# Kernel tuning notes

Hardware: AMD Instinct MI355X
Metric: run time of the kernel (lower is better)

Reference implementation:

```python
import jax, jax.numpy as jnp
import numpy as np

B, S, D, H, HD = 4, 2048, 1024, 16, 64  # batch, seq, d_model, heads, head_dim


def setup_inputs() -> dict:
    key = jax.random.key(0)
    ks = jax.random.split(key, 9)
    scale = 0.02
    x = jax.random.normal(ks[0], (B, S, D), jnp.float32)
    Wq = jax.random.normal(ks[1], (D, H, HD), jnp.float32) * scale
    Wk = jax.random.normal(ks[2], (D, H, HD), jnp.float32) * scale
    Wv = jax.random.normal(ks[3], (D, H, HD), jnp.float32) * scale
    bq = jax.random.normal(ks[4], (H, HD), jnp.float32) * scale
    bk = jax.random.normal(ks[5], (H, HD), jnp.float32) * scale
    bv = jax.random.normal(ks[6], (H, HD), jnp.float32) * scale
    Wo = jax.random.normal(ks[7], (H, HD, D), jnp.float32) * scale
    bo = jax.random.normal(ks[8], (D,), jnp.float32) * scale
    return {"x": x, "Wq": Wq, "bq": bq, "Wk": Wk, "bk": bk,
            "Wv": Wv, "bv": bv, "Wo": Wo, "bo": bo}


def reference(x, Wq, bq, Wk, bk, Wv, bv, Wo, bo):
    # QKV projections -> (B, S, H, HD)
    q = jnp.einsum("bsd,dhe->bshe", x, Wq) + bq
    k = jnp.einsum("bsd,dhe->bshe", x, Wk) + bk
    v = jnp.einsum("bsd,dhe->bshe", x, Wv) + bv
    # scaled dot-product attention (deterministic, no mask/bias)
    q = q / jnp.sqrt(jnp.asarray(HD, q.dtype))
    scores = jnp.einsum("bqhd,bkhd->bhqk", q, k)  # (B, H, S, S)
    attn = jax.nn.softmax(scores, axis=-1)
    ctx = jnp.einsum("bhqk,bkhd->bqhd", attn, v)  # (B, S, H, HD)
    # output projection -> (B, S, D)
    return jnp.einsum("bqhd,hdo->bqo", ctx, Wo) + bo
```

## Files before the change

### kernel.cpp

```cpp
#include <hip/hip_runtime.h>


typedef unsigned short u16;
typedef __attribute__((ext_vector_type(4))) float f32x4;
typedef __attribute__((ext_vector_type(8))) short s16x8;
typedef __attribute__((ext_vector_type(4))) unsigned short u16x4;
typedef __attribute__((ext_vector_type(4))) unsigned int u32x4;

#define DEV __device__ __forceinline__

#if __has_builtin(__builtin_amdgcn_exp2f)
#define EXP2(x) __builtin_amdgcn_exp2f(x)
#else
#define EXP2(x) exp2f(x)
#endif

DEV u16 f2b(float f) {
  unsigned u = __float_as_uint(f);
  u += 0x7fffu + ((u >> 16) & 1u);
  return (u16)(u >> 16);
}

DEV unsigned packb(float a, float b) {
  return (unsigned)f2b(a) | ((unsigned)f2b(b) << 16);
}

DEV void async16(const void* g, void* l) {
  __builtin_amdgcn_global_load_lds(
      (const __attribute__((address_space(1))) unsigned int*)g,
      (__attribute__((address_space(3))) unsigned int*)l, 16, 0, 0);
}

__global__ void k_cast(const float* __restrict__ x, u16* __restrict__ xb) {
  int i = (blockIdx.x * 256 + threadIdx.x) * 4;
  float4 v = *(const float4*)(x + i);
  u16x4 o;
  o.x = f2b(v.x); o.y = f2b(v.y); o.z = f2b(v.z); o.w = f2b(v.w);
  *(u16x4*)(xb + i) = o;
}

__global__ void k_packw(const float* __restrict__ src, u16* __restrict__ dst, float scale) {
  __shared__ float tile[32][33];
  int t = threadIdx.x;
  int k0 = blockIdx.x * 32, n0 = blockIdx.y * 32;
  int c = t & 31, r0 = t >> 5;
#pragma unroll
  for (int p = 0; p < 4; ++p) {
    int r = p * 8 + r0;
    tile[r][c] = src[(size_t)(k0 + r) * 1024 + n0 + c] * scale;
  }
  __syncthreads();
#pragma unroll
  for (int p = 0; p < 4; ++p) {
    int r = p * 8 + r0;
    dst[(size_t)(n0 + r) * 1024 + k0 + c] = f2b(tile[c][r]);
  }
}

__global__ void k_packbias(const float* __restrict__ bq, const float* __restrict__ bk,
                           const float* __restrict__ bv, float* __restrict__ out,
                           float qscale) {
  int t = blockIdx.x * 256 + threadIdx.x;
  float v = (t < 1024) ? bq[t] * qscale : (t < 2048 ? bk[t - 1024] : bv[t - 2048]);
  out[t] = v;
}

template <bool OUT_BF16>
__global__ __launch_bounds__(256, 2) void k_gemm_bt(
    const u16* __restrict__ A, const u16* __restrict__ Bt,
    const float* __restrict__ bias, void* __restrict__ Cout, u16* __restrict__ VT,
    int K, int ldC, int nsplit) {
  __shared__ u16 As[128 * 64];
  __shared__ u16 Bs[128 * 64];
  const int t = threadIdx.x;
  const int w = t >> 6, l = t & 63;
  const int lane15 = l & 15, quad = l >> 4;
  const int m0 = blockIdx.x * 128, n0 = blockIdx.y * 128;
  const int wm = (w >> 1) * 64, wn = (w & 1) * 64;

  const int srow = t >> 3, cp = t & 7;
  const u16* aSrc[4]; const u16* bSrc[4]; int ldsOff[4];
#pragma unroll
  for (int i = 0; i < 4; ++i) {
    int row = i * 32 + srow;
    int gc = cp ^ (row & 7);
    aSrc[i] = A + (size_t)(m0 + row) * K + gc * 8;
    bSrc[i] = Bt + (size_t)(n0 + row) * K + gc * 8;
    ldsOff[i] = (i * 32 + w * 8) * 64;
  }

  f32x4 acc[4][4] = {};

  for (int kk = 0; kk < K; kk += 64) {
#pragma unroll
    for (int i = 0; i < 4; ++i) async16(aSrc[i] + kk, As + ldsOff[i]);
#pragma unroll
    for (int i = 0; i < 4; ++i) async16(bSrc[i] + kk, Bs + ldsOff[i]);
    __builtin_amdgcn_s_waitcnt(0);
    __syncthreads();

#pragma unroll
    for (int ks = 0; ks < 2; ++ks) {
      s16x8 af[4], bf[4];
#pragma unroll
      for (int mi = 0; mi < 4; ++mi) {
        int r = wm + mi * 16 + lane15;
        int c = ks * 4 + quad;
        af[mi] = *(const s16x8*)(As + r * 64 + (c ^ (r & 7)) * 8);
      }
#pragma unroll
      for (int ni = 0; ni < 4; ++ni) {
        int r = wn + ni * 16 + lane15;
        int c = ks * 4 + quad;
        bf[ni] = *(const s16x8*)(Bs + r * 64 + (c ^ (r & 7)) * 8);
      }
#pragma unroll
      for (int mi = 0; mi < 4; ++mi)
#pragma unroll
        for (int ni = 0; ni < 4; ++ni)
          acc[mi][ni] = __builtin_amdgcn_mfma_f32_16x16x32_bf16(af[mi], bf[ni], acc[mi][ni], 0, 0, 0);
    }
    __syncthreads();
  }

  const bool vpath = (VT != nullptr) && (n0 >= nsplit);
#pragma unroll
  for (int ni = 0; ni < 4; ++ni) {
    int gn = n0 + wn + ni * 16 + lane15;
    float bb = bias[gn];
    if (!vpath) {
#pragma unroll
      for (int mi = 0; mi < 4; ++mi) {
        int gmBase = m0 + wm + mi * 16 + quad * 4;
#pragma unroll
        for (int r = 0; r < 4; ++r) {
          float v = acc[mi][ni][r] + bb;
          if (OUT_BF16)
            ((u16*)Cout)[(size_t)(gmBase + r) * ldC + gn] = f2b(v);
          else
            ((float*)Cout)[(size_t)(gmBase + r) * ldC + gn] = v;
        }
      }
    } else {
      int gv = gn - nsplit;
      int hh = gv >> 6, hd = gv & 63;
#pragma unroll
      for (int mi = 0; mi < 4; ++mi) {
        int gmBase = m0 + wm + mi * 16 + quad * 4;
        int bb2 = gmBase >> 11, s = gmBase & 2047;
        u16x4 o;
        o.x = f2b(acc[mi][ni][0] + bb);
        o.y = f2b(acc[mi][ni][1] + bb);
        o.z = f2b(acc[mi][ni][2] + bb);
        o.w = f2b(acc[mi][ni][3] + bb);
        *(u16x4*)(VT + (((size_t)(bb2 * 16 + hh) * 64 + hd) * 2048 + s)) = o;
      }
    }
  }
}

__global__ __launch_bounds__(256, 6) void k_flash(
    const u16* __restrict__ qkv, const u16* __restrict__ vt, u16* __restrict__ ctx) {
  __shared__ u16 Ks[64 * 64];
  __shared__ u16 Vs[64 * 64];
  const int t = threadIdx.x;
  const int w = t >> 6, l = t & 63;
  const int lane15 = l & 15, quad = l >> 4;
  const int qt = blockIdx.x, bh = blockIdx.y;
  const int b = bh >> 4, h = bh & 15;

  const int qrow = b * 2048 + qt * 64 + w * 16 + lane15;
  const u16* qp = qkv + (size_t)qrow * 2048 + h * 64 + quad * 8;
  s16x8 qf0 = *(const s16x8*)qp;
  s16x8 qf1 = *(const s16x8*)(qp + 32);

  const int srow = t >> 3, cp = t & 7;
  const u16* kSrc[2]; const u16* vSrc[2]; int ldsOff[2];
#pragma unroll
  for (int i = 0; i < 2; ++i) {
    int row = i * 32 + srow;
    int xk = (row & 3) | (((row >> 3) & 1) << 2);
    kSrc[i] = qkv + (size_t)(b * 2048 + row) * 2048 + 1024 + h * 64 + (cp ^ xk) * 8;
    vSrc[i] = vt + (size_t)bh * (64 * 2048) + (size_t)row * 2048 + (cp ^ (row & 7)) * 8;
    ldsOff[i] = (i * 32 + w * 8) * 64;
  }

  const int kr = (lane15 >> 2) * 8 + (lane15 & 3);
  f32x4 O[4] = {};
  float lacc = 0.f;

  for (int jt = 0; jt < 32; ++jt) {
    const size_t kAdv = (size_t)jt * 64 * 2048;
    const int vAdv = jt * 64;
#pragma unroll
    for (int i = 0; i < 2; ++i) async16(kSrc[i] + kAdv, Ks + ldsOff[i]);
#pragma unroll
    for (int i = 0; i < 2; ++i) async16(vSrc[i] + vAdv, Vs + ldsOff[i]);
    __builtin_amdgcn_s_waitcnt(0);
    __syncthreads();

    f32x4 st[4] = {};
#pragma unroll
    for (int ks = 0; ks < 2; ++ks) {
      s16x8 qf = ks ? qf1 : qf0;
#pragma unroll
      for (int tt = 0; tt < 4; ++tt) {
        int rr = kr + (tt & 1) * 4 + (tt >> 1) * 32;
        int xk = (rr & 3) | (((rr >> 3) & 1) << 2);
        s16x8 kf = *(const s16x8*)(Ks + rr * 64 + ((ks * 4 + quad) ^ xk) * 8);
        st[tt] = __builtin_amdgcn_mfma_f32_16x16x32_bf16(kf, qf, st[tt], 0, 0, 0);
      }
    }

    unsigned pr[4][2];
#pragma unroll
    for (int tt = 0; tt < 4; ++tt) {
      float p0 = EXP2(st[tt][0]), p1 = EXP2(st[tt][1]);
      float p2 = EXP2(st[tt][2]), p3 = EXP2(st[tt][3]);
      lacc += (p0 + p1) + (p2 + p3);
      pr[tt][0] = packb(p0, p1);
      pr[tt][1] = packb(p2, p3);
    }

#pragma unroll
    for (int ks = 0; ks < 2; ++ks) {
      u32x4 pu = {pr[2 * ks][0], pr[2 * ks][1], pr[2 * ks + 1][0], pr[2 * ks + 1][1]};
      s16x8 pf = __builtin_bit_cast(s16x8, pu);
#pragma unroll
      for (int co = 0; co < 4; ++co) {
        int rr = co * 16 + lane15;
        s16x8 vf = *(const s16x8*)(Vs + rr * 64 + ((ks * 4 + quad) ^ (rr & 7)) * 8);
        O[co] = __builtin_amdgcn_mfma_f32_16x16x32_bf16(vf, pf, O[co], 0, 0, 0);
      }
    }
    __syncthreads();
  }

  lacc += __shfl_xor(lacc, 16);
  lacc += __shfl_xor(lacc, 32);
  float inv = 1.0f / lacc;
#pragma unroll
  for (int co = 0; co < 4; ++co) {
    u16x4 o;
    o.x = f2b(O[co][0] * inv);
    o.y = f2b(O[co][1] * inv);
    o.z = f2b(O[co][2] * inv);
    o.w = f2b(O[co][3] * inv);
    *(u16x4*)(ctx + (size_t)qrow * 1024 + h * 64 + co * 16 + quad * 4) = o;
  }
}

static constexpr size_t OFF_XB  = 0;
static constexpr size_t OFF_WT  = OFF_XB + (16u << 20);
static constexpr size_t OFF_WOT = OFF_WT + (6u << 20);
static constexpr size_t OFF_B3  = OFF_WOT + (2u << 20);
static constexpr size_t OFF_QKV = OFF_B3 + (1u << 20);
static constexpr size_t OFF_VT  = OFF_QKV + (32u << 20);
static constexpr size_t OFF_CTX = OFF_VT + (16u << 20);

extern "C" void kernel_launch(void* const* d_in, const int* in_sizes, int n_in,
                              void* d_out, int out_size, void* d_ws, size_t ws_size,
                              hipStream_t stream) {
  const float* x  = (const float*)d_in[0];
  const float* Wq = (const float*)d_in[1];
  const float* bq = (const float*)d_in[2];
  const float* Wk = (const float*)d_in[3];
  const float* bk = (const float*)d_in[4];
  const float* Wv = (const float*)d_in[5];
  const float* bv = (const float*)d_in[6];
  const float* Wo = (const float*)d_in[7];
  const float* bo = (const float*)d_in[8];
  char* ws = (char*)d_ws;
  u16* xb    = (u16*)(ws + OFF_XB);
  u16* wt    = (u16*)(ws + OFF_WT);
  u16* wot   = (u16*)(ws + OFF_WOT);
  float* b3  = (float*)(ws + OFF_B3);
  u16* qkv   = (u16*)(ws + OFF_QKV);
  u16* vtb   = (u16*)(ws + OFF_VT);
  u16* ctx   = (u16*)(ws + OFF_CTX);
  float* out = (float*)d_out;

  const float QSCALE = 0.125f * 1.44269504f;

  k_cast<<<8192, 256, 0, stream>>>(x, xb);
  k_packw<<<dim3(32, 32), 256, 0, stream>>>(Wq, wt, QSCALE);
  k_packw<<<dim3(32, 32), 256, 0, stream>>>(Wk, wt + 1024 * 1024, 1.0f);
  k_packw<<<dim3(32, 32), 256, 0, stream>>>(Wv, wt + 2 * 1024 * 1024, 1.0f);
  k_packw<<<dim3(32, 32), 256, 0, stream>>>(Wo, wot, 1.0f);
  k_packbias<<<12, 256, 0, stream>>>(bq, bk, bv, b3, QSCALE);
  k_gemm_bt<true><<<dim3(64, 24), 256, 0, stream>>>(xb, wt, b3, qkv, vtb, 1024, 2048, 2048);
  k_flash<<<dim3(32, 64), 256, 0, stream>>>(qkv, vtb, ctx);
  k_gemm_bt<false><<<dim3(64, 8), 256, 0, stream>>>(ctx, wot, bo, out, nullptr, 1024, 1024, 1 << 30);
}
```

Baseline: 290.6 us.

## Enlarge flash KV tile, MFMA row sums, vectorized GEMM epilogues, merged weight packing

The attention kernel now processes 128 keys per iteration instead of 64, which halves the loop count and barrier pairs. The larger tile doubles LDS use and lowers the occupancy bound from 6 to 4. Softmax row sums are computed with an MFMA against a ones vector, replacing scalar adds and cross-lane shuffles. The GEMM swaps MFMA operand order so each lane holds four consecutive columns, giving vectorized bias loads and 8/16-byte stores. Other changes: the V-transpose path is split into its own launch, bf16 packing uses a hardware pack-convert when available, and the four weight-pack launches are merged into one.

```diff
diff --git a/kernel.cpp b/kernel.cpp
--- a/kernel.cpp
+++ b/kernel.cpp
@@ -5,6 +5,7 @@
 typedef __attribute__((ext_vector_type(4))) float f32x4;
 typedef __attribute__((ext_vector_type(8))) short s16x8;
 typedef __attribute__((ext_vector_type(4))) unsigned short u16x4;
+typedef __attribute__((ext_vector_type(2))) unsigned int u32x2;
 typedef __attribute__((ext_vector_type(4))) unsigned int u32x4;
 
 #define DEV __device__ __forceinline__
@@ -21,8 +22,14 @@
   return (u16)(u >> 16);
 }
 
-DEV unsigned packb(float a, float b) {
+DEV unsigned pack2(float a, float b) {
+#if __has_builtin(__builtin_amdgcn_cvt_pk_bf16_f32)
+  typedef __attribute__((ext_vector_type(2))) __bf16 bf16x2;
+  bf16x2 r = __builtin_amdgcn_cvt_pk_bf16_f32(a, b);
+  return __builtin_bit_cast(unsigned, r);
+#else
   return (unsigned)f2b(a) | ((unsigned)f2b(b) << 16);
+#endif
 }
 
 DEV void async16(const void* g, void* l) {
@@ -39,7 +46,16 @@
   *(u16x4*)(xb + i) = o;
 }
 
-__global__ void k_packw(const float* __restrict__ src, u16* __restrict__ dst, float scale) {
+__global__ void k_packw_all(const float* __restrict__ Wq, const float* __restrict__ Wk,
+                            const float* __restrict__ Wv, const float* __restrict__ Wo,
+                            u16* __restrict__ wt, u16* __restrict__ wot, float qscale) {
+  const float* src; u16* dst; float scale = 1.0f;
+  switch (blockIdx.z) {
+    case 0: src = Wq; dst = wt; scale = qscale; break;
+    case 1: src = Wk; dst = wt + 1024 * 1024; break;
+    case 2: src = Wv; dst = wt + 2 * 1024 * 1024; break;
+    default: src = Wo; dst = wot; break;
+  }
   __shared__ float tile[32][33];
   int t = threadIdx.x;
   int k0 = blockIdx.x * 32, n0 = blockIdx.y * 32;
@@ -65,17 +81,17 @@
   out[t] = v;
 }
 
-template <bool OUT_BF16>
+template <int MODE>
 __global__ __launch_bounds__(256, 2) void k_gemm_bt(
     const u16* __restrict__ A, const u16* __restrict__ Bt,
-    const float* __restrict__ bias, void* __restrict__ Cout, u16* __restrict__ VT,
-    int K, int ldC, int nsplit) {
+    const float* __restrict__ bias, void* __restrict__ Cout,
+    int K, int ldC, int nbase) {
   __shared__ u16 As[128 * 64];
   __shared__ u16 Bs[128 * 64];
   const int t = threadIdx.x;
   const int w = t >> 6, l = t & 63;
   const int lane15 = l & 15, quad = l >> 4;
-  const int m0 = blockIdx.x * 128, n0 = blockIdx.y * 128;
+  const int m0 = blockIdx.x * 128, n0 = nbase + blockIdx.y * 128;
   const int wm = (w >> 1) * 64, wn = (w & 1) * 64;
 
   const int srow = t >> 3, cp = t & 7;
@@ -118,51 +134,58 @@
       for (int mi = 0; mi < 4; ++mi)
 #pragma unroll
         for (int ni = 0; ni < 4; ++ni)
-          acc[mi][ni] = __builtin_amdgcn_mfma_f32_16x16x32_bf16(af[mi], bf[ni], acc[mi][ni], 0, 0, 0);
+          acc[mi][ni] = (MODE == 2)
+              ? __builtin_amdgcn_mfma_f32_16x16x32_bf16(af[mi], bf[ni], acc[mi][ni], 0, 0, 0)
+              : __builtin_amdgcn_mfma_f32_16x16x32_bf16(bf[ni], af[mi], acc[mi][ni], 0, 0, 0);
     }
     __syncthreads();
   }
 
-  const bool vpath = (VT != nullptr) && (n0 >= nsplit);
-#pragma unroll
-  for (int ni = 0; ni < 4; ++ni) {
-    int gn = n0 + wn + ni * 16 + lane15;
-    float bb = bias[gn];
-    if (!vpath) {
-#pragma unroll
-      for (int mi = 0; mi < 4; ++mi) {
-        int gmBase = m0 + wm + mi * 16 + quad * 4;
-#pragma unroll
-        for (int r = 0; r < 4; ++r) {
-          float v = acc[mi][ni][r] + bb;
-          if (OUT_BF16)
-            ((u16*)Cout)[(size_t)(gmBase + r) * ldC + gn] = f2b(v);
-          else
-            ((float*)Cout)[(size_t)(gmBase + r) * ldC + gn] = v;
-        }
-      }
-    } else {
-      int gv = gn - nsplit;
+  if (MODE == 2) {
+#pragma unroll
+    for (int ni = 0; ni < 4; ++ni) {
+      int gn = n0 + wn + ni * 16 + lane15;
+      float bb = bias[gn];
+      int gv = gn - 2048;
       int hh = gv >> 6, hd = gv & 63;
 #pragma unroll
       for (int mi = 0; mi < 4; ++mi) {
         int gmBase = m0 + wm + mi * 16 + quad * 4;
         int bb2 = gmBase >> 11, s = gmBase & 2047;
-        u16x4 o;
-        o.x = f2b(acc[mi][ni][0] + bb);
-        o.y = f2b(acc[mi][ni][1] + bb);
-        o.z = f2b(acc[mi][ni][2] + bb);
-        o.w = f2b(acc[mi][ni][3] + bb);
-        *(u16x4*)(VT + (((size_t)(bb2 * 16 + hh) * 64 + hd) * 2048 + s)) = o;
-      }
-    }
-  }
-}
-
-__global__ __launch_bounds__(256, 6) void k_flash(
+        u32x2 o;
+        o.x = pack2(acc[mi][ni][0] + bb, acc[mi][ni][1] + bb);
+        o.y = pack2(acc[mi][ni][2] + bb, acc[mi][ni][3] + bb);
+        *(u32x2*)((u16*)Cout + (((size_t)(bb2 * 16 + hh) * 64 + hd) * 2048 + s)) = o;
+      }
+    }
+  } else {
+#pragma unroll
+    for (int ni = 0; ni < 4; ++ni) {
+      int gnb = n0 + wn + ni * 16 + quad * 4;
+      float4 bb = *(const float4*)(bias + gnb);
+#pragma unroll
+      for (int mi = 0; mi < 4; ++mi) {
+        int gm = m0 + wm + mi * 16 + lane15;
+        if (MODE == 0) {
+          u32x2 o;
+          o.x = pack2(acc[mi][ni][0] + bb.x, acc[mi][ni][1] + bb.y);
+          o.y = pack2(acc[mi][ni][2] + bb.z, acc[mi][ni][3] + bb.w);
+          *(u32x2*)((u16*)Cout + (size_t)gm * ldC + gnb) = o;
+        } else {
+          float4 v;
+          v.x = acc[mi][ni][0] + bb.x; v.y = acc[mi][ni][1] + bb.y;
+          v.z = acc[mi][ni][2] + bb.z; v.w = acc[mi][ni][3] + bb.w;
+          *(float4*)((float*)Cout + (size_t)gm * ldC + gnb) = v;
+        }
+      }
+    }
+  }
+}
+
+__global__ __launch_bounds__(256, 4) void k_flash(
     const u16* __restrict__ qkv, const u16* __restrict__ vt, u16* __restrict__ ctx) {
-  __shared__ u16 Ks[64 * 64];
-  __shared__ u16 Vs[64 * 64];
+  __shared__ u16 Ks[128 * 64];
+  __shared__ u16 Vs[64 * 128];
   const int t = threadIdx.x;
   const int w = t >> 6, l = t & 63;
   const int lane15 = l & 15, quad = l >> 4;
@@ -175,78 +198,72 @@
   s16x8 qf1 = *(const s16x8*)(qp + 32);
 
   const int srow = t >> 3, cp = t & 7;
-  const u16* kSrc[2]; const u16* vSrc[2]; int ldsOff[2];
-#pragma unroll
-  for (int i = 0; i < 2; ++i) {
-    int row = i * 32 + srow;
-    int xk = (row & 3) | (((row >> 3) & 1) << 2);
-    kSrc[i] = qkv + (size_t)(b * 2048 + row) * 2048 + 1024 + h * 64 + (cp ^ xk) * 8;
-    vSrc[i] = vt + (size_t)bh * (64 * 2048) + (size_t)row * 2048 + (cp ^ (row & 7)) * 8;
+  const u16* kSrc[4]; const u16* vSrc[4]; int ldsOff[4];
+#pragma unroll
+  for (int i = 0; i < 4; ++i) {
+    int krow = i * 32 + srow;
+    int xk = (krow & 3) | (((krow >> 3) & 1) << 2);
+    kSrc[i] = qkv + (size_t)(b * 2048 + krow) * 2048 + 1024 + h * 64 + (cp ^ xk) * 8;
+    int vrow = i * 16 + w * 4 + quad;
+    vSrc[i] = vt + (size_t)bh * (64 * 2048) + (size_t)vrow * 2048 + (lane15 ^ (vrow & 7)) * 8;
     ldsOff[i] = (i * 32 + w * 8) * 64;
   }
 
   const int kr = (lane15 >> 2) * 8 + (lane15 & 3);
   f32x4 O[4] = {};
-  float lacc = 0.f;
-
-  for (int jt = 0; jt < 32; ++jt) {
-    const size_t kAdv = (size_t)jt * 64 * 2048;
-    const int vAdv = jt * 64;
-#pragma unroll
-    for (int i = 0; i < 2; ++i) async16(kSrc[i] + kAdv, Ks + ldsOff[i]);
-#pragma unroll
-    for (int i = 0; i < 2; ++i) async16(vSrc[i] + vAdv, Vs + ldsOff[i]);
+  f32x4 sacc = {};
+  const u32x4 onesu = {0x3F803F80u, 0x3F803F80u, 0x3F803F80u, 0x3F803F80u};
+  const s16x8 onesf = __builtin_bit_cast(s16x8, onesu);
+
+  for (int jt = 0; jt < 16; ++jt) {
+    const size_t kAdv = (size_t)jt * 128 * 2048;
+    const int vAdv = jt * 128;
+#pragma unroll
+    for (int i = 0; i < 4; ++i) async16(kSrc[i] + kAdv, Ks + ldsOff[i]);
+#pragma unroll
+    for (int i = 0; i < 4; ++i) async16(vSrc[i] + vAdv, Vs + ldsOff[i]);
     __builtin_amdgcn_s_waitcnt(0);
     __syncthreads();
 
-    f32x4 st[4] = {};
-#pragma unroll
-    for (int ks = 0; ks < 2; ++ks) {
-      s16x8 qf = ks ? qf1 : qf0;
-#pragma unroll
-      for (int tt = 0; tt < 4; ++tt) {
+    f32x4 st[8] = {};
+#pragma unroll
+    for (int ks2 = 0; ks2 < 2; ++ks2) {
+      s16x8 qf = ks2 ? qf1 : qf0;
+#pragma unroll
+      for (int tt = 0; tt < 8; ++tt) {
         int rr = kr + (tt & 1) * 4 + (tt >> 1) * 32;
         int xk = (rr & 3) | (((rr >> 3) & 1) << 2);
-        s16x8 kf = *(const s16x8*)(Ks + rr * 64 + ((ks * 4 + quad) ^ xk) * 8);
+        s16x8 kf = *(const s16x8*)(Ks + rr * 64 + ((ks2 * 4 + quad) ^ xk) * 8);
         st[tt] = __builtin_amdgcn_mfma_f32_16x16x32_bf16(kf, qf, st[tt], 0, 0, 0);
       }
     }
 
-    unsigned pr[4][2];
-#pragma unroll
-    for (int tt = 0; tt < 4; ++tt) {
-      float p0 = EXP2(st[tt][0]), p1 = EXP2(st[tt][1]);
-      float p2 = EXP2(st[tt][2]), p3 = EXP2(st[tt][3]);
-      lacc += (p0 + p1) + (p2 + p3);
-      pr[tt][0] = packb(p0, p1);
-      pr[tt][1] = packb(p2, p3);
-    }
-
-#pragma unroll
-    for (int ks = 0; ks < 2; ++ks) {
-      u32x4 pu = {pr[2 * ks][0], pr[2 * ks][1], pr[2 * ks + 1][0], pr[2 * ks + 1][1]};
+#pragma unroll
+    for (int ks = 0; ks < 4; ++ks) {
+      float p0 = EXP2(st[2 * ks][0]), p1 = EXP2(st[2 * ks][1]);
+      float p2 = EXP2(st[2 * ks][2]), p3 = EXP2(st[2 * ks][3]);
+      float p4 = EXP2(st[2 * ks + 1][0]), p5 = EXP2(st[2 * ks + 1][1]);
+      float p6 = EXP2(st[2 * ks + 1][2]), p7 = EXP2(st[2 * ks + 1][3]);
+      u32x4 pu = {pack2(p0, p1), pack2(p2, p3), pack2(p4, p5), pack2(p6, p7)};
       s16x8 pf = __builtin_bit_cast(s16x8, pu);
+      sacc = __builtin_amdgcn_mfma_f32_16x16x32_bf16(onesf, pf, sacc, 0, 0, 0);
 #pragma unroll
       for (int co = 0; co < 4; ++co) {
         int rr = co * 16 + lane15;
-        s16x8 vf = *(const s16x8*)(Vs + rr * 64 + ((ks * 4 + quad) ^ (rr & 7)) * 8);
+        s16x8 vf = *(const s16x8*)(Vs + rr * 128 + (((ks * 4 + quad) ^ (rr & 7))) * 8);
         O[co] = __builtin_amdgcn_mfma_f32_16x16x32_bf16(vf, pf, O[co], 0, 0, 0);
       }
     }
     __syncthreads();
   }
 
-  lacc += __shfl_xor(lacc, 16);
-  lacc += __shfl_xor(lacc, 32);
-  float inv = 1.0f / lacc;
+  float inv = 1.0f / sacc[0];
 #pragma unroll
   for (int co = 0; co < 4; ++co) {
-    u16x4 o;
-    o.x = f2b(O[co][0] * inv);
-    o.y = f2b(O[co][1] * inv);
-    o.z = f2b(O[co][2] * inv);
-    o.w = f2b(O[co][3] * inv);
-    *(u16x4*)(ctx + (size_t)qrow * 1024 + h * 64 + co * 16 + quad * 4) = o;
+    u32x2 o;
+    o.x = pack2(O[co][0] * inv, O[co][1] * inv);
+    o.y = pack2(O[co][2] * inv, O[co][3] * inv);
+    *(u32x2*)(ctx + (size_t)qrow * 1024 + h * 64 + co * 16 + quad * 4) = o;
   }
 }
 
@@ -283,12 +300,10 @@
   const float QSCALE = 0.125f * 1.44269504f;
 
   k_cast<<<8192, 256, 0, stream>>>(x, xb);
-  k_packw<<<dim3(32, 32), 256, 0, stream>>>(Wq, wt, QSCALE);
-  k_packw<<<dim3(32, 32), 256, 0, stream>>>(Wk, wt + 1024 * 1024, 1.0f);
-  k_packw<<<dim3(32, 32), 256, 0, stream>>>(Wv, wt + 2 * 1024 * 1024, 1.0f);
-  k_packw<<<dim3(32, 32), 256, 0, stream>>>(Wo, wot, 1.0f);
+  k_packw_all<<<dim3(32, 32, 4), 256, 0, stream>>>(Wq, Wk, Wv, Wo, wt, wot, QSCALE);
   k_packbias<<<12, 256, 0, stream>>>(bq, bk, bv, b3, QSCALE);
-  k_gemm_bt<true><<<dim3(64, 24), 256, 0, stream>>>(xb, wt, b3, qkv, vtb, 1024, 2048, 2048);
+  k_gemm_bt<0><<<dim3(64, 16), 256, 0, stream>>>(xb, wt, b3, qkv, 1024, 2048, 0);
+  k_gemm_bt<2><<<dim3(64, 8), 256, 0, stream>>>(xb, wt, b3, vtb, 1024, 2048, 2048);
   k_flash<<<dim3(32, 64), 256, 0, stream>>>(qkv, vtb, ctx);
-  k_gemm_bt<false><<<dim3(64, 8), 256, 0, stream>>>(ctx, wot, bo, out, nullptr, 1024, 1024, 1 << 30);
-}
+  k_gemm_bt<1><<<dim3(64, 8), 256, 0, stream>>>(ctx, wot, bo, out, 1024, 1024, 0);
+}
```

After: 292.2 us. About the same (+0.5%).
